# Optimization experiments

Measured on AMD Instinct MI355X. Metric: run time of the kernel, lower is better.

Reference implementation:

```python
import jax, jax.numpy as jnp
import numpy as np

B, L, D, H, E, K = 16, 197, 768, 12, 8, 2
HID = 4 * D
HD = D // H
SCALE = HD ** -0.5
EPS = 1e-5


def _layernorm(x, g, b):
    m = jnp.mean(x, axis=-1, keepdims=True)
    v = jnp.mean((x - m) ** 2, axis=-1, keepdims=True)
    return (x - m) * jax.lax.rsqrt(v + EPS) * g + b


def setup_inputs() -> dict:
    key = jax.random.key(0)
    ks = jax.random.split(key, 8)
    s = 0.02
    return {
        "x": jax.random.normal(ks[0], (B, L, D), jnp.float32),
        "ln1_g": jnp.ones((D,), jnp.float32),
        "ln1_b": jnp.zeros((D,), jnp.float32),
        "qkv_w": jax.random.normal(ks[1], (D, 3 * D), jnp.float32) * s,
        "qkv_b": jnp.zeros((3 * D,), jnp.float32),
        "proj_w": jax.random.normal(ks[2], (D, D), jnp.float32) * s,
        "proj_b": jnp.zeros((D,), jnp.float32),
        "ln2_g": jnp.ones((D,), jnp.float32),
        "ln2_b": jnp.zeros((D,), jnp.float32),
        "w_gate": jax.random.normal(ks[3], (D, E), jnp.float32) * s,
        "w1": jax.random.normal(ks[4], (E, D, HID), jnp.float32) * s,
        "b1": jnp.zeros((E, HID), jnp.float32),
        "w2": jax.random.normal(ks[5], (E, HID, D), jnp.float32) * s,
        "b2": jnp.zeros((E, D), jnp.float32),
    }


def reference(x, ln1_g, ln1_b, qkv_w, qkv_b, proj_w, proj_b,
              ln2_g, ln2_b, w_gate, w1, b1, w2, b2):
    # --- attention branch: x = x + attn(norm1(x)) ---
    h = _layernorm(x, ln1_g, ln1_b)
    qkv = (h @ qkv_w + qkv_b).reshape(B, L, 3, H, HD)
    q, k, v = [qkv[:, :, i].transpose(0, 2, 1, 3) for i in range(3)]  # [B,H,L,HD]
    attn = jax.nn.softmax(jnp.einsum('bhqd,bhkd->bhqk', q, k) * SCALE, axis=-1)
    o = jnp.einsum('bhqk,bhkd->bhqd', attn, v).transpose(0, 2, 1, 3).reshape(B, L, D)
    x = x + o @ proj_w + proj_b

    # --- MoE FFN branch on norm2(x), tokens flattened ---
    flat = _layernorm(x, ln2_g, ln2_b).reshape(-1, D)  # [T, D], T = B*L
    T = flat.shape[0]
    # noisy top-k gating, eval path (no noise): top-(k+1) logits, softmax over top-k
    logits = flat @ w_gate                              # [T, E]
    top_vals, top_idx = jax.lax.top_k(logits, K + 1)
    probs = jax.nn.softmax(top_vals[:, :K], axis=-1)    # [T, K]
    gates = jnp.zeros((T, E), flat.dtype).at[
        jnp.arange(T)[:, None], top_idx[:, :K]].set(probs)  # sparse gate matrix

    # dense equivalent of SparseDispatcher dispatch -> expert MLP -> combine:
    # output[t] = sum_e gates[t,e] * (gelu(flat @ w1[e] + b1[e]) @ w2[e] + b2[e])
    hid = jax.nn.gelu(jnp.einsum('td,edf->tef', flat, w1) + b1, approximate=False)
    y = jnp.einsum('te,tef,efd->td', gates, hid, w2) + gates @ b2
    return x + y.reshape(B, L, D)
```

## Files before the change

kernel.cpp:

```cpp
#include <hip/hip_runtime.h>
#include <math.h>
#include <stdint.h>

typedef unsigned short u16;
typedef unsigned int u32;
typedef float floatx4 __attribute__((ext_vector_type(4)));
typedef __bf16 bf16x8 __attribute__((ext_vector_type(8)));

#define T_TOK 3152
#define SEQ 197
#define NH 12
#define LISTN 7424
#define MOE_MT 58
#define YHALF ((size_t)LISTN * 768)

__device__ __forceinline__ float bf2f(u16 u) { return __uint_as_float(((u32)u) << 16); }
__device__ __forceinline__ u16 f2bf(float f) {
    u32 u = __float_as_uint(f);
    u += 0x7FFFu + ((u >> 16) & 1u);
    return (u16)(u >> 16);
}
__device__ __forceinline__ float wred_sum(float v) {
#pragma unroll
    for (int off = 32; off; off >>= 1) v += __shfl_xor(v, off);
    return v;
}

__device__ __forceinline__ float gelu_fast(float v) {
    float x = fabsf(v) * 0.70710678118654752f;
    float t = __builtin_amdgcn_rcpf(fmaf(0.3275911f, x, 1.0f));
    float p = t * fmaf(t, fmaf(t, fmaf(t, fmaf(t, 1.061405429f, -1.453152027f),
                                       1.421413741f), -0.284496736f), 0.254829592f);
    float er = fmaf(-p, __expf(-x * x), 1.0f);
    er = copysignf(er, v);
    return 0.5f * v * (1.0f + er);
}

#define GLB_AS(p) ((const __attribute__((address_space(1))) void*)(uintptr_t)(p))
#define LDS_AS(p) ((__attribute__((address_space(3))) void*)(uintptr_t)(p))
__device__ __forceinline__ void gl_lds16(const u16* g, u16* l) {
    __builtin_amdgcn_global_load_lds(GLB_AS(g), LDS_AS(l), 16, 0, 0);
}

template <int SPLIT>
__global__ __launch_bounds__(256) void transp_kernel(const float* __restrict__ in,
        u16* __restrict__ oh, u16* __restrict__ ol, int R, int C) {
    int r0 = blockIdx.x * 64, c0 = blockIdx.y * 64;
    size_t zo = (size_t)blockIdx.z * R * C;
    __shared__ float Lt[64][68];
    int tid = threadIdx.x;
    int rr = tid >> 2, cs = (tid & 3) * 16;
    const float* src = in + zo + (size_t)(r0 + rr) * C + c0 + cs;
#pragma unroll
    for (int i = 0; i < 4; i++) *(float4*)&Lt[rr][cs + i * 4] = *(const float4*)(src + i * 4);
    __syncthreads();
    int cw = tid >> 2, rs = (tid & 3) * 16;
    u16 hv[16], lv[16];
#pragma unroll
    for (int j = 0; j < 16; j++) {
        float v = Lt[rs + j][cw];
        u16 hb = f2bf(v);
        hv[j] = hb;
        if (SPLIT) lv[j] = f2bf(v - bf2f(hb));
    }
    u16* dst = oh + zo + (size_t)(c0 + cw) * R + r0 + rs;
    *(uint4*)dst = *(const uint4*)&hv[0];
    *(uint4*)(dst + 8) = *(const uint4*)&hv[8];
    if (SPLIT) {
        u16* dstl = ol + zo + (size_t)(c0 + cw) * R + r0 + rs;
        *(uint4*)dstl = *(const uint4*)&lv[0];
        *(uint4*)(dstl + 8) = *(const uint4*)&lv[8];
    }
}

__global__ __launch_bounds__(256) void ln1_kernel(const float* __restrict__ x,
        const float* __restrict__ g, const float* __restrict__ b,
        u16* __restrict__ h_hi, u16* __restrict__ h_lo) {
    int t = blockIdx.x, tid = threadIdx.x;
    int w = tid >> 6, lane = tid & 63;
    float v[3];
#pragma unroll
    for (int i = 0; i < 3; i++) v[i] = x[(size_t)t * 768 + tid + i * 256];
    float s = v[0] + v[1] + v[2];
    float q = v[0] * v[0] + v[1] * v[1] + v[2] * v[2];
    s = wred_sum(s); q = wred_sum(q);
    __shared__ float red[8];
    if (lane == 0) { red[w] = s; red[4 + w] = q; }
    __syncthreads();
    float st = red[0] + red[1] + red[2] + red[3];
    float qt = red[4] + red[5] + red[6] + red[7];
    float mean = st * (1.f / 768.f);
    float var = qt * (1.f / 768.f) - mean * mean;
    float rs = rsqrtf(var + 1e-5f);
#pragma unroll
    for (int i = 0; i < 3; i++) {
        int d = tid + i * 256;
        float hv = (v[i] - mean) * rs * g[d] + b[d];
        u16 hi = f2bf(hv);
        h_hi[(size_t)t * 768 + d] = hi;
        h_lo[(size_t)t * 768 + d] = f2bf(hv - bf2f(hi));
    }
}

template <int MODE>
__global__ __launch_bounds__(256) void gemm128(const u16* __restrict__ Ah,
        const u16* __restrict__ Al, const u16* __restrict__ Bh, const u16* __restrict__ Bl,
        const float* __restrict__ bias, void* __restrict__ Cv, const float* __restrict__ resid,
        const int* __restrict__ list, const int* __restrict__ asg, int M, int N, int K) {
    constexpr bool SPLIT = (MODE <= 1);
    int m0 = blockIdx.x * 128, n0 = blockIdx.y * 128;
    const u16* Bph = Bh;
    const u16* Bpl = Bl;
    const float* bp = bias;
    if (MODE >= 2) {
        if (m0 >= asg[8]) return;
        int e = 0;
        while (m0 >= asg[e + 1]) ++e;
        Bph = Bh + (size_t)e * N * K;
        bp = bias + (size_t)e * N;
    }
    int kbeg = 0, kend = K;
    if (MODE == 3) { int kh = K >> 1; kbeg = blockIdx.z * kh; kend = kbeg + kh; }

    __shared__ u16 Ash[2 * 4096];
    __shared__ u16 Bsh[2 * 4096];
    __shared__ u16 Asl[SPLIT ? 2 * 4096 : 64];
    __shared__ u16 Bsl[SPLIT ? 2 * 4096 : 64];

    int tid = threadIdx.x;
    int w = tid >> 6, lane = tid & 63, l15 = lane & 15, quad = lane >> 4;
    int wm = (w & 1) * 64, wn = (w >> 1) * 64;
    int lr = lane >> 2;
    int lc = ((lane & 3) ^ ((lane >> 3) & 3)) * 8;

    const u16* ga[2]; const u16* gal[2];
    const u16* gb[2]; const u16* gbl[2];
    int ldro[2];
#pragma unroll
    for (int it = 0; it < 2; it++) {
        int arow = m0 + it * 64 + w * 16 + lr;
        if (MODE == 2) {
            int entry = list[arow];
            ga[it] = Ah + (size_t)(entry >= 0 ? (entry >> 1) : 0) * K + lc;
        } else if (MODE == 3) {
            ga[it] = Ah + (size_t)arow * K + lc;
        } else {
            int rc = min(arow, M - 1);
            ga[it] = Ah + (size_t)rc * K + lc;
            gal[it] = Al + (size_t)rc * K + lc;
        }
        int brow = n0 + it * 64 + w * 16 + lr;
        gb[it] = Bph + (size_t)brow * K + lc;
        if (SPLIT) gbl[it] = Bpl + (size_t)brow * K + lc;
        ldro[it] = (it * 64 + w * 16) * 32;
    }

    int ra[4], rb[4];
#pragma unroll
    for (int i = 0; i < 4; i++) {
        int r1 = wm + i * 16 + l15;
        ra[i] = r1 * 32 + (quad ^ ((r1 >> 1) & 3)) * 8;
        int r2 = wn + i * 16 + l15;
        rb[i] = r2 * 32 + (quad ^ ((r2 >> 1) & 3)) * 8;
    }

    floatx4 acc[4][4];
#pragma unroll
    for (int mi = 0; mi < 4; mi++)
#pragma unroll
        for (int ni = 0; ni < 4; ni++) acc[mi][ni] = (floatx4){0.f, 0.f, 0.f, 0.f};

    auto stage = [&](int buf, int k0) {
        int bo = buf * 4096;
#pragma unroll
        for (int it = 0; it < 2; it++) {
            gl_lds16(ga[it] + k0, &Ash[bo + ldro[it]]);
            gl_lds16(gb[it] + k0, &Bsh[bo + ldro[it]]);
            if constexpr (SPLIT) {
                gl_lds16(gal[it] + k0, &Asl[bo + ldro[it]]);
                gl_lds16(gbl[it] + k0, &Bsl[bo + ldro[it]]);
            }
        }
    };
    auto compute = [&](int buf) {
        int bo = buf * 4096;
        bf16x8 afh[4], bfh[4], afl[4], bfl[4];
#pragma unroll
        for (int i = 0; i < 4; i++) {
            afh[i] = *(const bf16x8*)&Ash[bo + ra[i]];
            bfh[i] = *(const bf16x8*)&Bsh[bo + rb[i]];
            if constexpr (SPLIT) {
                afl[i] = *(const bf16x8*)&Asl[bo + ra[i]];
                bfl[i] = *(const bf16x8*)&Bsl[bo + rb[i]];
            }
        }
#pragma unroll
        for (int mi = 0; mi < 4; mi++)
#pragma unroll
            for (int ni = 0; ni < 4; ni++) {
                if constexpr (SPLIT) {
                    acc[mi][ni] = __builtin_amdgcn_mfma_f32_16x16x32_bf16(afl[mi], bfh[ni], acc[mi][ni], 0, 0, 0);
                    acc[mi][ni] = __builtin_amdgcn_mfma_f32_16x16x32_bf16(afh[mi], bfl[ni], acc[mi][ni], 0, 0, 0);
                }
                acc[mi][ni] = __builtin_amdgcn_mfma_f32_16x16x32_bf16(afh[mi], bfh[ni], acc[mi][ni], 0, 0, 0);
            }
    };

    int nsteps = (kend - kbeg) >> 5;
    stage(0, kbeg);
    __syncthreads();
    for (int s = 0; s < nsteps; s += 2) {
        int k0 = kbeg + s * 32;
        stage(1, k0 + 32);
        compute(0);
        __syncthreads();
        if (s + 2 < nsteps) stage(0, k0 + 64);
        compute(1);
        __syncthreads();
    }

    float* Cf = (float*)Cv;
    if (MODE == 3) Cf += (size_t)blockIdx.z * ((size_t)M * N);
#pragma unroll
    for (int ni = 0; ni < 4; ni++) {
        int col = n0 + wn + ni * 16 + l15;
        float bb = bp[col];
        if (MODE == 3 && blockIdx.z != 0) bb = 0.f;
#pragma unroll
        for (int mi = 0; mi < 4; mi++) {
#pragma unroll
            for (int r = 0; r < 4; r++) {
                int row = m0 + wm + mi * 16 + quad * 4 + r;
                float v = acc[mi][ni][r] + bb;
                if (MODE == 0) {
                    if (row < M) Cf[(size_t)row * N + col] = v;
                } else if (MODE == 1) {
                    if (row < M) Cf[(size_t)row * N + col] = v + resid[(size_t)row * N + col];
                } else if (MODE == 2) {
                    if (list[row] >= 0) {
                        ((u16*)Cv)[(size_t)row * N + col] = f2bf(gelu_fast(v));
                    }
                } else {
                    if (list[row] >= 0) Cf[(size_t)row * N + col] = v;
                }
            }
        }
    }
}

__global__ __launch_bounds__(256) void attn_mfma_kernel(const float* __restrict__ qkv,
        u16* __restrict__ ohi, u16* __restrict__ olo) {
    int by = blockIdx.y;
    int b = by / NH, h = by % NH;
    int qbase = blockIdx.x * 64;
    int tid = threadIdx.x;
    int w = tid >> 6, lane = tid & 63, l15 = lane & 15, quad = lane >> 4;

    __shared__ u16 Qh[64 * 72], Ql[64 * 72];
    __shared__ u16 Sh[64 * 72], Sl[64 * 72];
    __shared__ u16 Ph[64 * 72], Pl[64 * 72];

    int srow = tid >> 2;
    int scol = (tid & 3) * 16;

    {
        int qr = min(qbase + srow, SEQ - 1);
        const float* src = qkv + ((size_t)(b * SEQ + qr)) * 2304 + h * 64 + scol;
        u16 hv[16], lv[16];
#pragma unroll
        for (int i = 0; i < 4; i++) {
            float4 v = *(const float4*)(src + i * 4);
            float vv[4] = {v.x, v.y, v.z, v.w};
#pragma unroll
            for (int j = 0; j < 4; j++) {
                u16 hb = f2bf(vv[j]);
                hv[i * 4 + j] = hb;
                lv[i * 4 + j] = f2bf(vv[j] - bf2f(hb));
            }
        }
        int o = srow * 72 + scol;
        *(uint4*)&Qh[o] = *(const uint4*)&hv[0];
        *(uint4*)&Qh[o + 8] = *(const uint4*)&hv[8];
        *(uint4*)&Ql[o] = *(const uint4*)&lv[0];
        *(uint4*)&Ql[o + 8] = *(const uint4*)&lv[8];
    }
    __syncthreads();
    bf16x8 aqh[2], aql[2];
#pragma unroll
    for (int s2 = 0; s2 < 2; s2++) {
        aqh[s2] = *(const bf16x8*)&Qh[(w * 16 + l15) * 72 + s2 * 32 + quad * 8];
        aql[s2] = *(const bf16x8*)&Ql[(w * 16 + l15) * 72 + s2 * 32 + quad * 8];
    }
    __syncthreads();

    floatx4 sc[16];
#pragma unroll
    for (int f = 0; f < 16; f++) sc[f] = (floatx4){0.f, 0.f, 0.f, 0.f};

    for (int t = 0; t < 4; t++) {
        int key = t * 64 + srow;
        u16 hv[16], lv[16];
        if (key < SEQ) {
            const float* src = qkv + ((size_t)(b * SEQ + key)) * 2304 + 768 + h * 64 + scol;
#pragma unroll
            for (int i = 0; i < 4; i++) {
                float4 v = *(const float4*)(src + i * 4);
                float vv[4] = {v.x, v.y, v.z, v.w};
#pragma unroll
                for (int j = 0; j < 4; j++) {
                    u16 hb = f2bf(vv[j]);
                    hv[i * 4 + j] = hb;
                    lv[i * 4 + j] = f2bf(vv[j] - bf2f(hb));
                }
            }
        } else {
#pragma unroll
            for (int i = 0; i < 16; i++) { hv[i] = 0; lv[i] = 0; }
        }
        int o = srow * 72 + scol;
        *(uint4*)&Sh[o] = *(const uint4*)&hv[0];
        *(uint4*)&Sh[o + 8] = *(const uint4*)&hv[8];
        *(uint4*)&Sl[o] = *(const uint4*)&lv[0];
        *(uint4*)&Sl[o + 8] = *(const uint4*)&lv[8];
        __syncthreads();
#pragma unroll
        for (int s = 0; s < 4; s++) {
#pragma unroll
            for (int s2 = 0; s2 < 2; s2++) {
                bf16x8 bkh = *(const bf16x8*)&Sh[(s * 16 + l15) * 72 + s2 * 32 + quad * 8];
                bf16x8 bkl = *(const bf16x8*)&Sl[(s * 16 + l15) * 72 + s2 * 32 + quad * 8];
                sc[t * 4 + s] = __builtin_amdgcn_mfma_f32_16x16x32_bf16(aql[s2], bkh, sc[t * 4 + s], 0, 0, 0);
                sc[t * 4 + s] = __builtin_amdgcn_mfma_f32_16x16x32_bf16(aqh[s2], bkl, sc[t * 4 + s], 0, 0, 0);
                sc[t * 4 + s] = __builtin_amdgcn_mfma_f32_16x16x32_bf16(aqh[s2], bkh, sc[t * 4 + s], 0, 0, 0);
            }
        }
        __syncthreads();
    }

    float m[4] = {-1e30f, -1e30f, -1e30f, -1e30f};
#pragma unroll
    for (int f = 0; f < 16; f++) {
        int key = (f >> 2) * 64 + (f & 3) * 16 + l15;
        bool valid = key < SEQ;
#pragma unroll
        for (int r = 0; r < 4; r++) {
            float s = valid ? sc[f][r] * 0.125f : -1e30f;
            sc[f][r] = s;
            m[r] = fmaxf(m[r], s);
        }
    }
#pragma unroll
    for (int r = 0; r < 4; r++) {
#pragma unroll
        for (int off = 1; off < 16; off <<= 1) m[r] = fmaxf(m[r], __shfl_xor(m[r], off));
    }
    float sum[4] = {0.f, 0.f, 0.f, 0.f};
#pragma unroll
    for (int f = 0; f < 16; f++) {
#pragma unroll
        for (int r = 0; r < 4; r++) {
            float p = expf(sc[f][r] - m[r]);
            sc[f][r] = p;
            sum[r] += p;
        }
    }
    float inv[4];
#pragma unroll
    for (int r = 0; r < 4; r++) {
#pragma unroll
        for (int off = 1; off < 16; off <<= 1) sum[r] += __shfl_xor(sum[r], off);
        inv[r] = 1.f / sum[r];
    }

    floatx4 oacc[4];
#pragma unroll
    for (int sd = 0; sd < 4; sd++) oacc[sd] = (floatx4){0.f, 0.f, 0.f, 0.f};

    for (int t = 0; t < 4; t++) {
#pragma unroll
        for (int s = 0; s < 4; s++) {
#pragma unroll
            for (int r = 0; r < 4; r++) {
                float p = sc[t * 4 + s][r];
                u16 hb = f2bf(p);
                int row = w * 16 + quad * 4 + r;
                Ph[row * 72 + s * 16 + l15] = hb;
                Pl[row * 72 + s * 16 + l15] = f2bf(p - bf2f(hb));
            }
        }
        {
            int key = t * 64 + srow;
            float vv[16];
            if (key < SEQ) {
                const float* src = qkv + ((size_t)(b * SEQ + key)) * 2304 + 1536 + h * 64 + scol;
#pragma unroll
                for (int i = 0; i < 4; i++) {
                    float4 v = *(const float4*)(src + i * 4);
                    vv[i * 4 + 0] = v.x; vv[i * 4 + 1] = v.y; vv[i * 4 + 2] = v.z; vv[i * 4 + 3] = v.w;
                }
            } else {
#pragma unroll
                for (int i = 0; i < 16; i++) vv[i] = 0.f;
            }
#pragma unroll
            for (int i = 0; i < 16; i++) {
                u16 hb = f2bf(vv[i]);
                Sh[(scol + i) * 72 + srow] = hb;
                Sl[(scol + i) * 72 + srow] = f2bf(vv[i] - bf2f(hb));
            }
        }
        __syncthreads();
#pragma unroll
        for (int s2 = 0; s2 < 2; s2++) {
            bf16x8 aph = *(const bf16x8*)&Ph[(w * 16 + l15) * 72 + s2 * 32 + quad * 8];
            bf16x8 apl = *(const bf16x8*)&Pl[(w * 16 + l15) * 72 + s2 * 32 + quad * 8];
#pragma unroll
            for (int sd = 0; sd < 4; sd++) {
                bf16x8 bvh = *(const bf16x8*)&Sh[(sd * 16 + l15) * 72 + s2 * 32 + quad * 8];
                bf16x8 bvl = *(const bf16x8*)&Sl[(sd * 16 + l15) * 72 + s2 * 32 + quad * 8];
                oacc[sd] = __builtin_amdgcn_mfma_f32_16x16x32_bf16(apl, bvh, oacc[sd], 0, 0, 0);
                oacc[sd] = __builtin_amdgcn_mfma_f32_16x16x32_bf16(aph, bvl, oacc[sd], 0, 0, 0);
                oacc[sd] = __builtin_amdgcn_mfma_f32_16x16x32_bf16(aph, bvh, oacc[sd], 0, 0, 0);
            }
        }
        __syncthreads();
    }

#pragma unroll
    for (int sd = 0; sd < 4; sd++) {
#pragma unroll
        for (int r = 0; r < 4; r++) {
            int q = qbase + w * 16 + quad * 4 + r;
            if (q < SEQ) {
                float val = oacc[sd][r] * inv[r];
                u16 hb = f2bf(val);
                size_t o = ((size_t)(b * SEQ + q)) * 768 + h * 64 + sd * 16 + l15;
                ohi[o] = hb;
                olo[o] = f2bf(val - bf2f(hb));
            }
        }
    }
}

__global__ __launch_bounds__(256) void ln2_gate_kernel(const float* __restrict__ x1,
        const float* __restrict__ g, const float* __restrict__ b, const float* __restrict__ wg,
        u16* __restrict__ flat, int2* __restrict__ idx, float2* __restrict__ gate) {
    int t = blockIdx.x, tid = threadIdx.x;
    int w = tid >> 6, lane = tid & 63;
    float v[3];
#pragma unroll
    for (int i = 0; i < 3; i++) v[i] = x1[(size_t)t * 768 + tid + i * 256];
    float s = v[0] + v[1] + v[2];
    float q = v[0] * v[0] + v[1] * v[1] + v[2] * v[2];
    s = wred_sum(s); q = wred_sum(q);
    __shared__ float red[8];
    __shared__ float fs[768];
    __shared__ float lg[8];
    if (lane == 0) { red[w] = s; red[4 + w] = q; }
    __syncthreads();
    float st = red[0] + red[1] + red[2] + red[3];
    float qt = red[4] + red[5] + red[6] + red[7];
    float mean = st * (1.f / 768.f);
    float var = qt * (1.f / 768.f) - mean * mean;
    float rs = rsqrtf(var + 1e-5f);
#pragma unroll
    for (int i = 0; i < 3; i++) {
        int d = tid + i * 256;
        float f = (v[i] - mean) * rs * g[d] + b[d];
        flat[(size_t)t * 768 + d] = f2bf(f);
        fs[d] = f;
    }
    __syncthreads();
    int e0 = 2 * w, e1 = 2 * w + 1;
    float p0 = 0.f, p1 = 0.f;
    for (int d = lane; d < 768; d += 64) {
        float f = fs[d];
        p0 += f * wg[d * 8 + e0];
        p1 += f * wg[d * 8 + e1];
    }
    p0 = wred_sum(p0); p1 = wred_sum(p1);
    if (lane == 0) { lg[e0] = p0; lg[e1] = p1; }
    __syncthreads();
    if (tid == 0) {
        float b0 = -1e30f, b1 = -1e30f;
        int i0 = 0, i1 = 0;
        for (int e = 0; e < 8; e++) {
            float le = lg[e];
            if (le > b0) { b1 = b0; i1 = i0; b0 = le; i0 = e; }
            else if (le > b1) { b1 = le; i1 = e; }
        }
        float ex = expf(b1 - b0);
        float den = 1.f + ex;
        idx[t] = make_int2(i0, i1);
        gate[t] = make_float2(1.f / den, ex / den);
    }
}

__global__ __launch_bounds__(256) void hist_kernel(const int2* __restrict__ idx, int* __restrict__ cnt) {
    int t = blockIdx.x * 256 + threadIdx.x;
    if (t < T_TOK) {
        int2 id = idx[t];
        atomicAdd(&cnt[id.x], 1);
        atomicAdd(&cnt[id.y], 1);
    }
}

__global__ void offsets_kernel(const int* __restrict__ cnt, int* __restrict__ asg) {
    if (threadIdx.x == 0 && blockIdx.x == 0) {
        int acc = 0;
        asg[0] = 0;
        for (int e = 0; e < 8; e++) { acc += (cnt[e] + 127) & ~127; asg[e + 1] = acc; }
    }
}

__global__ __launch_bounds__(256) void scatter_kernel(const int2* __restrict__ idx,
        const int* __restrict__ asg, int* __restrict__ cursor,
        int* __restrict__ list, int* __restrict__ pos) {
    int t = blockIdx.x * 256 + threadIdx.x;
    if (t >= T_TOK) return;
    int2 id = idx[t];
    int p0 = asg[id.x] + atomicAdd(&cursor[id.x], 1);
    list[p0] = t * 2;
    pos[t * 2] = p0;
    int p1 = asg[id.y] + atomicAdd(&cursor[id.y], 1);
    list[p1] = t * 2 + 1;
    pos[t * 2 + 1] = p1;
}

__global__ __launch_bounds__(256) void final_kernel(const float* __restrict__ x1,
        const float* __restrict__ yp, const int* __restrict__ pos,
        const float2* __restrict__ gate, float* __restrict__ out) {
    int t = blockIdx.x, tid = threadIdx.x;
    float2 g = gate[t];
    int p0 = pos[t * 2], p1 = pos[t * 2 + 1];
#pragma unroll
    for (int i = 0; i < 3; i++) {
        int d = tid + i * 256;
        float y0 = yp[(size_t)p0 * 768 + d] + yp[YHALF + (size_t)p0 * 768 + d];
        float y1 = yp[(size_t)p1 * 768 + d] + yp[YHALF + (size_t)p1 * 768 + d];
        out[(size_t)t * 768 + d] = x1[(size_t)t * 768 + d] + g.x * y0 + g.y * y1;
    }
}

extern "C" void kernel_launch(void* const* d_in, const int* in_sizes, int n_in,
                              void* d_out, int out_size, void* d_ws, size_t ws_size,
                              hipStream_t stream) {
    const float* x      = (const float*)d_in[0];
    const float* ln1_g  = (const float*)d_in[1];
    const float* ln1_b  = (const float*)d_in[2];
    const float* qkv_w  = (const float*)d_in[3];
    const float* qkv_b  = (const float*)d_in[4];
    const float* proj_w = (const float*)d_in[5];
    const float* proj_b = (const float*)d_in[6];
    const float* ln2_g  = (const float*)d_in[7];
    const float* ln2_b  = (const float*)d_in[8];
    const float* w_gate = (const float*)d_in[9];
    const float* w1     = (const float*)d_in[10];
    const float* b1     = (const float*)d_in[11];
    const float* w2     = (const float*)d_in[12];
    const float* b2     = (const float*)d_in[13];

    char* ws = (char*)d_ws;
    size_t off = 0;
    auto alloc = [&](size_t bytes) { size_t cur = off; off = (off + bytes + 255) & ~(size_t)255; return cur; };
    u16*    h_hi  = (u16*)   (ws + alloc((size_t)T_TOK * 768 * 2));
    u16*    h_lo  = (u16*)   (ws + alloc((size_t)T_TOK * 768 * 2));
    float*  qkvf  = (float*) (ws + alloc((size_t)T_TOK * 2304 * 4));
    u16*    o_hi  = (u16*)   (ws + alloc((size_t)T_TOK * 768 * 2));
    u16*    o_lo  = (u16*)   (ws + alloc((size_t)T_TOK * 768 * 2));
    float*  ypair = (float*) ws;
    float*  x1    = (float*) (ws + alloc((size_t)T_TOK * 768 * 4));
    u16*    flat  = (u16*)   (ws + alloc((size_t)T_TOK * 768 * 2));
    int2*   idx   = (int2*)  (ws + alloc((size_t)T_TOK * 8));
    float2* gate  = (float2*)(ws + alloc((size_t)T_TOK * 8));
    int*    cnt   = (int*)   (ws + alloc(64));
    int*    cursor = cnt + 8;
    int*    asg   = (int*)   (ws + alloc(64));
    int*    list  = (int*)   (ws + alloc((size_t)LISTN * 4));
    int*    pos   = (int*)   (ws + alloc((size_t)T_TOK * 2 * 4));
    u16*    hid   = (u16*)   (ws + alloc((size_t)LISTN * 3072 * 2));
    u16*    qkvt_h = (u16*)  (ws + alloc((size_t)2304 * 768 * 2));
    u16*    qkvt_l = (u16*)  (ws + alloc((size_t)2304 * 768 * 2));
    u16*    projt_h = (u16*) (ws + alloc((size_t)768 * 768 * 2));
    u16*    projt_l = (u16*) (ws + alloc((size_t)768 * 768 * 2));
    u16*    w1t   = (u16*)   (ws + alloc((size_t)8 * 3072 * 768 * 2));
    u16*    w2t   = (u16*)   (ws + alloc((size_t)8 * 768 * 3072 * 2));

    hipMemsetAsync(cnt, 0, 64, stream);
    hipMemsetAsync(list, 0xFF, (size_t)LISTN * 4, stream);

    transp_kernel<1><<<dim3(12, 36, 1), 256, 0, stream>>>(qkv_w, qkvt_h, qkvt_l, 768, 2304);
    transp_kernel<1><<<dim3(12, 12, 1), 256, 0, stream>>>(proj_w, projt_h, projt_l, 768, 768);
    transp_kernel<0><<<dim3(12, 48, 8), 256, 0, stream>>>(w1, w1t, nullptr, 768, 3072);
    transp_kernel<0><<<dim3(48, 12, 8), 256, 0, stream>>>(w2, w2t, nullptr, 3072, 768);

    ln1_kernel<<<T_TOK, 256, 0, stream>>>(x, ln1_g, ln1_b, h_hi, h_lo);
    gemm128<0><<<dim3(25, 18), 256, 0, stream>>>(h_hi, h_lo, qkvt_h, qkvt_l, qkv_b, qkvf,
                                                 nullptr, nullptr, nullptr, T_TOK, 2304, 768);
    attn_mfma_kernel<<<dim3(4, 192), 256, 0, stream>>>(qkvf, o_hi, o_lo);
    gemm128<1><<<dim3(25, 6), 256, 0, stream>>>(o_hi, o_lo, projt_h, projt_l, proj_b, x1,
                                                x, nullptr, nullptr, T_TOK, 768, 768);
    ln2_gate_kernel<<<T_TOK, 256, 0, stream>>>(x1, ln2_g, ln2_b, w_gate, flat, idx, gate);
    hist_kernel<<<(T_TOK + 255) / 256, 256, 0, stream>>>(idx, cnt);
    offsets_kernel<<<1, 64, 0, stream>>>(cnt, asg);
    scatter_kernel<<<(T_TOK + 255) / 256, 256, 0, stream>>>(idx, asg, cursor, list, pos);
    gemm128<2><<<dim3(MOE_MT, 24), 256, 0, stream>>>(flat, nullptr, w1t, nullptr, b1, hid,
                                                     nullptr, list, asg, LISTN, 3072, 768);
    gemm128<3><<<dim3(MOE_MT, 6, 2), 256, 0, stream>>>(hid, nullptr, w2t, nullptr, b2, ypair,
                                                       nullptr, list, asg, LISTN, 768, 3072);
    final_kernel<<<T_TOK, 256, 0, stream>>>(x1, ypair, pos, gate, (float*)d_out);
}
```

Measured before the change: 611.9 us.

## Remap GEMM block IDs across XCDs and stage MoE hidden stores through LDS

Block indices are remapped so that consecutive logical tiles (same M row-tile, adjacent N tiles) land on the same XCD, which is meant to improve L2 reuse of the A operand on the chiplet-based GPU. For the expert up-projection (MODE 2), the GELU bf16 output is first written to swizzled shared memory and then stored as coalesced 16-byte rows, replacing scattered 2-byte global stores. Shared arrays are merged into one buffer so the epilogue can reuse it. The remap hardcodes grid dimensions per mode, which must match the launch configuration.

New measurement: 570.2 us. 6.8% less time.

```diff
diff --git a/kernel.cpp b/kernel.cpp
--- a/kernel.cpp
+++ b/kernel.cpp
@@ -108,10 +108,23 @@
         const float* __restrict__ bias, void* __restrict__ Cv, const float* __restrict__ resid,
         const int* __restrict__ list, const int* __restrict__ asg, int M, int N, int K) {
     constexpr bool SPLIT = (MODE <= 1);
-    int m0 = blockIdx.x * 128, n0 = blockIdx.y * 128;
+    constexpr int GX = (MODE <= 1) ? 25 : MOE_MT;
+    constexpr int GY = (MODE == 0) ? 18 : (MODE == 2) ? 24 : 6;
+    constexpr int GZ = (MODE == 3) ? 2 : 1;
+    constexpr int G  = GX * GY * GZ;
+    constexpr int NT = GY * GZ;
+    constexpr int Q8 = G >> 3, R8 = G & 7;
+
+    int d = blockIdx.x + GX * (blockIdx.y + GY * blockIdx.z);
+    int j = d & 7, s = d >> 3;
+    int v = (j < R8) ? (j * (Q8 + 1) + s) : (R8 * (Q8 + 1) + (j - R8) * Q8 + s);
+    int mt = v / NT, nzr = v - mt * NT;
+    int yt = nzr % GY, zt = nzr / GY;
+    int m0 = mt * 128, n0 = yt * 128;
+
     const u16* Bph = Bh;
+    const float* bp = bias;
     const u16* Bpl = Bl;
-    const float* bp = bias;
     if (MODE >= 2) {
         if (m0 >= asg[8]) return;
         int e = 0;
@@ -120,12 +133,13 @@
         bp = bias + (size_t)e * N;
     }
     int kbeg = 0, kend = K;
-    if (MODE == 3) { int kh = K >> 1; kbeg = blockIdx.z * kh; kend = kbeg + kh; }
-
-    __shared__ u16 Ash[2 * 4096];
-    __shared__ u16 Bsh[2 * 4096];
-    __shared__ u16 Asl[SPLIT ? 2 * 4096 : 64];
-    __shared__ u16 Bsl[SPLIT ? 2 * 4096 : 64];
+    if (MODE == 3) { int kh = K >> 1; kbeg = zt * kh; kend = kbeg + kh; }
+
+    __shared__ __align__(16) u16 SM[SPLIT ? 32768 : 16384];
+    u16* Ash = SM;
+    u16* Bsh = SM + 8192;
+    u16* Asl = SPLIT ? SM + 16384 : SM;
+    u16* Bsl = SPLIT ? SM + 24576 : SM;
 
     int tid = threadIdx.x;
     int w = tid >> 6, lane = tid & 63, l15 = lane & 15, quad = lane >> 4;
@@ -209,39 +223,65 @@
     int nsteps = (kend - kbeg) >> 5;
     stage(0, kbeg);
     __syncthreads();
-    for (int s = 0; s < nsteps; s += 2) {
-        int k0 = kbeg + s * 32;
+    for (int s2 = 0; s2 < nsteps; s2 += 2) {
+        int k0 = kbeg + s2 * 32;
         stage(1, k0 + 32);
         compute(0);
         __syncthreads();
-        if (s + 2 < nsteps) stage(0, k0 + 64);
+        if (s2 + 2 < nsteps) stage(0, k0 + 64);
         compute(1);
         __syncthreads();
     }
 
+    if constexpr (MODE == 2) {
+#pragma unroll
+        for (int ni = 0; ni < 4; ni++) {
+            int col = wn + ni * 16 + l15;
+            float bb = bp[n0 + col];
+#pragma unroll
+            for (int mi = 0; mi < 4; mi++) {
+#pragma unroll
+                for (int r = 0; r < 4; r++) {
+                    int row = wm + mi * 16 + quad * 4 + r;
+                    float gv = gelu_fast(acc[mi][ni][r] + bb);
+                    SM[row * 128 + (col ^ ((row & 7) << 3))] = f2bf(gv);
+                }
+            }
+        }
+        __syncthreads();
+        int rr = tid >> 1, half = (tid & 1) * 64;
+        int grow = m0 + rr;
+        if (list[grow] >= 0) {
+            u16* dst = (u16*)Cv + (size_t)grow * N + n0 + half;
+            int xr = (rr & 7) << 3;
+#pragma unroll
+            for (int gch = 0; gch < 8; gch++) {
+                int cb = (half + gch * 8) ^ xr;
+                *(uint4*)(dst + gch * 8) = *(const uint4*)&SM[rr * 128 + cb];
+            }
+        }
+        return;
+    }
+
     float* Cf = (float*)Cv;
-    if (MODE == 3) Cf += (size_t)blockIdx.z * ((size_t)M * N);
+    if (MODE == 3) Cf += (size_t)zt * ((size_t)M * N);
 #pragma unroll
     for (int ni = 0; ni < 4; ni++) {
         int col = n0 + wn + ni * 16 + l15;
         float bb = bp[col];
-        if (MODE == 3 && blockIdx.z != 0) bb = 0.f;
+        if (MODE == 3 && zt != 0) bb = 0.f;
 #pragma unroll
         for (int mi = 0; mi < 4; mi++) {
 #pragma unroll
             for (int r = 0; r < 4; r++) {
                 int row = m0 + wm + mi * 16 + quad * 4 + r;
-                float v = acc[mi][ni][r] + bb;
+                float v2 = acc[mi][ni][r] + bb;
                 if (MODE == 0) {
-                    if (row < M) Cf[(size_t)row * N + col] = v;
+                    if (row < M) Cf[(size_t)row * N + col] = v2;
                 } else if (MODE == 1) {
-                    if (row < M) Cf[(size_t)row * N + col] = v + resid[(size_t)row * N + col];
-                } else if (MODE == 2) {
-                    if (list[row] >= 0) {
-                        ((u16*)Cv)[(size_t)row * N + col] = f2bf(gelu_fast(v));
-                    }
+                    if (row < M) Cf[(size_t)row * N + col] = v2 + resid[(size_t)row * N + col];
                 } else {
-                    if (list[row] >= 0) Cf[(size_t)row * N + col] = v;
+                    if (list[row] >= 0) Cf[(size_t)row * N + col] = v2;
                 }
             }
         }
```
